# Kernel optimization log

Hardware: AMD Instinct MI355X
Metric: run time of the kernel (lower is better)

## Reference

```python
import jax, jax.numpy as jnp
import numpy as np

DIM = 128      # encoder output dim
D_OUT = 10     # num classes
T = 1.0        # temperature
EPS = 1e-7


def setup_inputs() -> dict:
    key = jax.random.key(0)
    ks = jax.random.split(key, 5)
    B, N, D_IN = 512, 100000, 128
    x = jax.random.normal(ks[0], (B, D_IN), jnp.float32)
    candidate_x = jax.random.normal(ks[1], (N, D_IN), jnp.float32)
    candidate_y = jax.random.randint(ks[2], (N,), 0, D_OUT, dtype=jnp.int32)
    W = jax.random.normal(ks[3], (DIM, D_IN), jnp.float32) / np.sqrt(D_IN).astype(np.float32)
    b = jax.random.normal(ks[4], (DIM,), jnp.float32) * 0.01
    return {"x": x, "candidate_x": candidate_x, "candidate_y": candidate_y, "W": W, "b": b}


def reference(x, candidate_x, candidate_y, W, b):
    # Linear encoder (n_blocks == 0 path)
    h = x @ W.T + b              # [B, DIM]
    hc = candidate_x @ W.T + b   # [N, DIM]
    # Pairwise L2 distances via the Gram expansion (same math as torch.cdist p=2)
    d2 = (jnp.sum(h * h, axis=-1, keepdims=True)
          + jnp.sum(hc * hc, axis=-1)[None, :]
          - 2.0 * (h @ hc.T))    # [B, N]
    dist = jnp.sqrt(jnp.maximum(d2, 0.0)) / T
    # Attention-like masked softmax over candidates (eval: no diagonal mask)
    p = jax.nn.softmax(-dist, axis=-1)              # [B, N]
    onehot_y = jax.nn.one_hot(candidate_y, D_OUT, dtype=p.dtype)  # [N, D_OUT]
    logits = p @ onehot_y                           # [B, D_OUT]
    return jnp.log(logits + EPS)
```

## Files before the change

kernel.cpp:

```cpp
#include <hip/hip_runtime.h>
#include <stdint.h>

typedef __bf16 bf16x8 __attribute__((ext_vector_type(8)));
typedef float f32x4 __attribute__((ext_vector_type(4)));
typedef short short8 __attribute__((ext_vector_type(8)));
typedef unsigned short ushort4v __attribute__((ext_vector_type(4)));
typedef float float4_t __attribute__((ext_vector_type(4)));

union FragU { short8 s; bf16x8 b; };

#define DEVI static __device__ __forceinline__

DEVI f32x4 mfma16(bf16x8 a, bf16x8 b, f32x4 c) {
  return __builtin_amdgcn_mfma_f32_16x16x32_bf16(a, b, c, 0, 0, 0);
}

DEVI bf16x8 cvt8(float4_t a, float4_t b) {
  bf16x8 r;
  r[0] = (__bf16)a[0]; r[1] = (__bf16)a[1]; r[2] = (__bf16)a[2]; r[3] = (__bf16)a[3];
  r[4] = (__bf16)b[0]; r[5] = (__bf16)b[1]; r[6] = (__bf16)b[2]; r[7] = (__bf16)b[3];
  return r;
}

__global__ __launch_bounds__(256) void setup_kernel(
    const float* __restrict__ W, unsigned short* __restrict__ Wbf,
    const int* __restrict__ y, unsigned short* __restrict__ YT,
    float* __restrict__ hcn, int N, int NP, int bpc) {
  const int bid = blockIdx.x, t = threadIdx.x;
  if (bid < 8) {
    int i = (bid * 256 + t) * 8;
    float4_t v0 = *(const float4_t*)(W + i);
    float4_t v1 = *(const float4_t*)(W + i + 4);
    FragU u; u.b = cvt8(v0, v1);
    *(short8*)(Wbf + i) = u.s;
  } else if (bid == 8) {
    int i = N + t;
    if (i < NP) hcn[i] = 1e30f;
  } else {
    int k = bid - 9;
    int c = k / bpc, j = k - c * bpc;
    int n0 = j * 2048 + t * 8;
    unsigned short* dst = YT + (size_t)c * NP + n0;
#pragma unroll
    for (int e = 0; e < 8; ++e) {
      int n = n0 + e;
      if (n < NP) dst[e] = (n < N && y[n] == c) ? 0x3F80u : 0u;
    }
  }
}

__global__ __launch_bounds__(256) void encode_kernel(
    const float* __restrict__ in, const unsigned short* __restrict__ Wbf,
    const float* __restrict__ bias, unsigned short* __restrict__ outh,
    float* __restrict__ outnorm, int M) {
  const int t = threadIdx.x, lane = t & 63, w = t >> 6;
  const int g = lane >> 4, q = lane & 15;
  const int rowbase = blockIdx.x * 64 + w * 16;

  bf16x8 a[4];
  {
    int arow = rowbase + q;
    bool v = arow < M;
    int ar = v ? arow : 0;
#pragma unroll
    for (int kc = 0; kc < 4; ++kc) {
      const float4_t* p = (const float4_t*)(in + (size_t)ar * 128 + kc * 32 + g * 8);
      float4_t v0 = p[0], v1 = p[1];
      FragU u; u.b = cvt8(v0, v1);
      if (!v) u.s = short8{0, 0, 0, 0, 0, 0, 0, 0};
      a[kc] = u.b;
    }
  }

  f32x4 acc[8];
#pragma unroll
  for (int nt = 0; nt < 8; ++nt) acc[nt] = f32x4{0.f, 0.f, 0.f, 0.f};

#pragma unroll
  for (int nt = 0; nt < 8; ++nt) {
#pragma unroll
    for (int kc = 0; kc < 4; ++kc) {
      FragU u;
      u.s = *(const short8*)(Wbf + (size_t)(nt * 16 + q) * 128 + kc * 32 + g * 8);
      acc[nt] = mfma16(a[kc], u.b, acc[nt]);
    }
  }

  float nsq[4] = {0.f, 0.f, 0.f, 0.f};
#pragma unroll
  for (int nt = 0; nt < 8; ++nt) {
    int col = nt * 16 + q;
    float bv = bias[col];
#pragma unroll
    for (int r = 0; r < 4; ++r) {
      int row = rowbase + g * 4 + r;
      float val = acc[nt][r] + bv;
      __bf16 h = (__bf16)val;
      float vf = (float)h;
      nsq[r] += vf * vf;
      union { __bf16 h; unsigned short u; } cv; cv.h = h;
      if (row < M) outh[(size_t)row * 128 + col] = cv.u;
    }
  }
#pragma unroll
  for (int m = 1; m < 16; m <<= 1) {
#pragma unroll
    for (int r = 0; r < 4; ++r) nsq[r] += __shfl_xor(nsq[r], m, 64);
  }
  if (q == 0) {
#pragma unroll
    for (int r = 0; r < 4; ++r) {
      int row = rowbase + g * 4 + r;
      if (row < M) outnorm[row] = nsq[r];
    }
  }
}

__global__ __launch_bounds__(512) void nca_main(
    const unsigned short* __restrict__ H, const float* __restrict__ hnorm,
    const unsigned short* __restrict__ HC, const float* __restrict__ hcnorm,
    const unsigned short* __restrict__ YT, float* __restrict__ gbins,
    int B, int N, int NP, int NT, int CHUNKS) {
  __shared__ __align__(16) unsigned short HCl[2][64 * 128];

  const int t = threadIdx.x, lane = t & 63, w = t >> 6;
  const int g = lane >> 4, q = lane & 15;
  const int rg = blockIdx.y, chunk = blockIdx.x;
  const int t0 = (int)(((long long)chunk * NT) / CHUNKS);
  const int t1 = (int)(((long long)(chunk + 1) * NT) / CHUNKS);
  const int rowbase = rg * 128 + w * 16;

  bf16x8 hfrag[4];
  {
    int arow = rowbase + q;
    bool v = arow < B;
    int ar = v ? arow : 0;
#pragma unroll
    for (int kc = 0; kc < 4; ++kc) {
      FragU u;
      u.s = *(const short8*)(H + (size_t)ar * 128 + kc * 32 + g * 8);
      if (!v) u.s = short8{0, 0, 0, 0, 0, 0, 0, 0};
      hfrag[kc] = u.b;
    }
  }
  const int hrow = rowbase + q;
  const float hn = hnorm[hrow < B ? hrow : 0];

  f32x4 pool = f32x4{0.f, 0.f, 0.f, 0.f};

#define STAGE(TT, BUF)                                                        \
  {                                                                           \
    _Pragma("unroll") for (int i = 0; i < 2; ++i) {                           \
      int SI = t + 512 * i;                                                   \
      int row = SI >> 4, s = SI & 15;                                         \
      int srcslot = s ^ (row & 7);                                            \
      int cg = (TT)*64 + row;                                                 \
      if (cg >= N) cg = N - 1;                                                \
      const unsigned short* src = HC + (size_t)cg * 128 + srcslot * 8;        \
      char* ldsbase = (char*)HCl[BUF] + w * 1024 + i * 8192;                  \
      __builtin_amdgcn_global_load_lds(                                       \
          (const __attribute__((address_space(1))) unsigned int*)src,         \
          (__attribute__((address_space(3))) unsigned int*)ldsbase, 16, 0, 0);\
    }                                                                         \
  }

  int cur = 0;
  if (t0 < t1) STAGE(t0, 0);

  for (int tt = t0; tt < t1; ++tt) {
    __syncthreads();
    if (tt + 1 < t1) STAGE(tt + 1, cur ^ 1);

    const int colbase = tt * 64;
    float4_t cnv[4];
    ushort4v ytv[4];
#pragma unroll
    for (int ns = 0; ns < 4; ++ns) {
      cnv[ns] = *(const float4_t*)(hcnorm + colbase + ns * 16 + g * 4);
      ytv[ns] = *(const ushort4v*)(YT + (size_t)q * NP + colbase + ns * 16 + g * 4);
    }

    f32x4 acc[4];
#pragma unroll
    for (int ns = 0; ns < 4; ++ns) acc[ns] = f32x4{0.f, 0.f, 0.f, 0.f};
#pragma unroll
    for (int ns = 0; ns < 4; ++ns) {
      int brow = ns * 16 + q;
#pragma unroll
      for (int kc = 0; kc < 4; ++kc) {
        int slot = (kc * 4 + g) ^ (brow & 7);
        FragU u;
        u.s = *(const short8*)((const char*)HCl[cur] + brow * 256 + slot * 16);
        acc[ns] = mfma16(u.b, hfrag[kc], acc[ns]);
      }
    }

#pragma unroll
    for (int ns = 0; ns < 4; ++ns) {
      FragU wb; wb.s = short8{0, 0, 0, 0, 0, 0, 0, 0};
#pragma unroll
      for (int r = 0; r < 4; ++r) {
        float d2 = fmaf(-2.f, acc[ns][r], hn + cnv[ns][r]);
        d2 = fmaxf(d2, 0.f);
        float dist = __builtin_amdgcn_sqrtf(d2);
        wb.b[r] = (__bf16)__expf(0.f - dist);
      }
      FragU yb;
      yb.s = short8{(short)ytv[ns][0], (short)ytv[ns][1],
                    (short)ytv[ns][2], (short)ytv[ns][3], 0, 0, 0, 0};
      pool = mfma16(yb.b, wb.b, pool);
    }
    cur ^= 1;
  }

  if (hrow < B) {
#pragma unroll
    for (int r = 0; r < 4; ++r) {
      int c = g * 4 + r;
      if (c < 10) atomicAdd(&gbins[hrow * 10 + c], pool[r]);
    }
  }
#undef STAGE
}

__global__ __launch_bounds__(256) void finalize_kernel(
    const float* __restrict__ gbins, float* __restrict__ out, int B) {
  int row = blockIdx.x * blockDim.x + threadIdx.x;
  if (row >= B) return;
  float s[10], Z = 0.f;
#pragma unroll
  for (int c = 0; c < 10; ++c) {
    s[c] = gbins[row * 10 + c];
    Z += s[c];
  }
  float inv = 1.f / Z;
#pragma unroll
  for (int c = 0; c < 10; ++c) out[row * 10 + c] = logf(fmaf(s[c], inv, 1e-7f));
}

extern "C" void kernel_launch(void* const* d_in, const int* in_sizes, int n_in,
                              void* d_out, int out_size, void* d_ws,
                              size_t ws_size, hipStream_t stream) {
  const float* x = (const float*)d_in[0];
  const float* cx = (const float*)d_in[1];
  const int* cy = (const int*)d_in[2];
  const float* W = (const float*)d_in[3];
  const float* b = (const float*)d_in[4];
  const int B = in_sizes[0] / 128;
  const int N = in_sizes[1] / 128;
  float* out = (float*)d_out;

  const int NT = (N + 63) / 64;
  const int NP = NT * 64;

  char* ws = (char*)d_ws;
  size_t o = 0;
  auto alloc = [&](size_t bytes) {
    size_t r = o;
    o += (bytes + 255) & ~(size_t)255;
    return r;
  };
  unsigned short* HC = (unsigned short*)(ws + alloc((size_t)N * 128 * 2));
  float* hcn = (float*)(ws + alloc((size_t)NP * 4));
  unsigned short* H = (unsigned short*)(ws + alloc((size_t)B * 128 * 2));
  float* hn = (float*)(ws + alloc((size_t)B * 4));
  float* gbins = (float*)(ws + alloc((size_t)B * 10 * 4));
  unsigned short* Wbf = (unsigned short*)(ws + alloc(128 * 128 * 2));
  unsigned short* YT = (unsigned short*)(ws + alloc((size_t)16 * NP * 2));

  (void)hipMemsetAsync(gbins, 0, (size_t)B * 10 * 4, stream);
  const int bpc = (NP + 2047) / 2048;
  setup_kernel<<<9 + 16 * bpc, 256, 0, stream>>>(W, Wbf, cy, YT, hcn, N, NP, bpc);
  encode_kernel<<<(N + 63) / 64, 256, 0, stream>>>(cx, Wbf, b, HC, hcn, N);
  encode_kernel<<<(B + 63) / 64, 256, 0, stream>>>(x, Wbf, b, H, hn, B);

  const int CHUNKS = 192;
  const int RG = (B + 127) / 128;
  dim3 grid(CHUNKS, RG);
  nca_main<<<grid, 512, 0, stream>>>(H, hn, HC, hcn, YT, gbins, B, N, NP, NT,
                                     CHUNKS);
  finalize_kernel<<<(B + 255) / 256, 256, 0, stream>>>(gbins, out, B);
}
```

Measured before the change: 201.5 us.

## Process two query row-sets per block and replace atomics with partial-sum reduction

```diff
diff --git a/kernel.cpp b/kernel.cpp
--- a/kernel.cpp
+++ b/kernel.cpp
@@ -4,10 +4,11 @@
 typedef __bf16 bf16x8 __attribute__((ext_vector_type(8)));
 typedef float f32x4 __attribute__((ext_vector_type(4)));
 typedef short short8 __attribute__((ext_vector_type(8)));
-typedef unsigned short ushort4v __attribute__((ext_vector_type(4)));
+typedef unsigned int uint2v __attribute__((ext_vector_type(2)));
 typedef float float4_t __attribute__((ext_vector_type(4)));
 
 union FragU { short8 s; bf16x8 b; };
+union YbU { uint2v u2[2]; bf16x8 b; };
 
 #define DEVI static __device__ __forceinline__
 
@@ -50,12 +51,23 @@
 }
 
 __global__ __launch_bounds__(256) void encode_kernel(
-    const float* __restrict__ in, const unsigned short* __restrict__ Wbf,
-    const float* __restrict__ bias, unsigned short* __restrict__ outh,
-    float* __restrict__ outnorm, int M) {
+    const float* __restrict__ inA, const float* __restrict__ inB,
+    const unsigned short* __restrict__ Wbf, const float* __restrict__ bias,
+    unsigned short* __restrict__ outA, float* __restrict__ normA,
+    unsigned short* __restrict__ outB, float* __restrict__ normB,
+    int MA, int MB, int NBA) {
+  const float* in;
+  unsigned short* outh;
+  float* outnorm;
+  int M, blk;
+  if ((int)blockIdx.x < NBA) {
+    in = inA; outh = outA; outnorm = normA; M = MA; blk = blockIdx.x;
+  } else {
+    in = inB; outh = outB; outnorm = normB; M = MB; blk = blockIdx.x - NBA;
+  }
   const int t = threadIdx.x, lane = t & 63, w = t >> 6;
   const int g = lane >> 4, q = lane & 15;
-  const int rowbase = blockIdx.x * 64 + w * 16;
+  const int rowbase = blk * 64 + w * 16;
 
   bf16x8 a[4];
   {
@@ -75,7 +87,6 @@
   f32x4 acc[8];
 #pragma unroll
   for (int nt = 0; nt < 8; ++nt) acc[nt] = f32x4{0.f, 0.f, 0.f, 0.f};
-
 #pragma unroll
   for (int nt = 0; nt < 8; ++nt) {
 #pragma unroll
@@ -116,11 +127,11 @@
   }
 }
 
-__global__ __launch_bounds__(512) void nca_main(
+__global__ __launch_bounds__(512, 4) void nca_main(
     const unsigned short* __restrict__ H, const float* __restrict__ hnorm,
     const unsigned short* __restrict__ HC, const float* __restrict__ hcnorm,
-    const unsigned short* __restrict__ YT, float* __restrict__ gbins,
-    int B, int N, int NP, int NT, int CHUNKS) {
+    const unsigned short* __restrict__ YT, float* __restrict__ part,
+    int B, int BP, int N, int NP, int NT, int CHUNKS) {
   __shared__ __align__(16) unsigned short HCl[2][64 * 128];
 
   const int t = threadIdx.x, lane = t & 63, w = t >> 6;
@@ -128,25 +139,27 @@
   const int rg = blockIdx.y, chunk = blockIdx.x;
   const int t0 = (int)(((long long)chunk * NT) / CHUNKS);
   const int t1 = (int)(((long long)(chunk + 1) * NT) / CHUNKS);
-  const int rowbase = rg * 128 + w * 16;
-
-  bf16x8 hfrag[4];
-  {
-    int arow = rowbase + q;
-    bool v = arow < B;
-    int ar = v ? arow : 0;
+
+  bf16x8 hfrag[2][4];
+  float hn[2];
+  int hrow[2];
+#pragma unroll
+  for (int s = 0; s < 2; ++s) {
+    hrow[s] = rg * 256 + s * 128 + w * 16 + q;
+    bool v = hrow[s] < B;
+    int ar = v ? hrow[s] : 0;
 #pragma unroll
     for (int kc = 0; kc < 4; ++kc) {
       FragU u;
       u.s = *(const short8*)(H + (size_t)ar * 128 + kc * 32 + g * 8);
       if (!v) u.s = short8{0, 0, 0, 0, 0, 0, 0, 0};
-      hfrag[kc] = u.b;
-    }
-  }
-  const int hrow = rowbase + q;
-  const float hn = hnorm[hrow < B ? hrow : 0];
-
-  f32x4 pool = f32x4{0.f, 0.f, 0.f, 0.f};
+      hfrag[s][kc] = u.b;
+    }
+    hn[s] = hnorm[ar];
+  }
+
+  f32x4 pool0 = f32x4{0.f, 0.f, 0.f, 0.f};
+  f32x4 pool1 = f32x4{0.f, 0.f, 0.f, 0.f};
 
 #define STAGE(TT, BUF)                                                        \
   {                                                                           \
@@ -173,69 +186,70 @@
 
     const int colbase = tt * 64;
     float4_t cnv[4];
-    ushort4v ytv[4];
+    uint2v ytu[4];
 #pragma unroll
     for (int ns = 0; ns < 4; ++ns) {
       cnv[ns] = *(const float4_t*)(hcnorm + colbase + ns * 16 + g * 4);
-      ytv[ns] = *(const ushort4v*)(YT + (size_t)q * NP + colbase + ns * 16 + g * 4);
-    }
-
-    f32x4 acc[4];
-#pragma unroll
-    for (int ns = 0; ns < 4; ++ns) acc[ns] = f32x4{0.f, 0.f, 0.f, 0.f};
+      ytu[ns] = *(const uint2v*)(YT + (size_t)q * NP + colbase + ns * 16 + g * 4);
+    }
+
 #pragma unroll
     for (int ns = 0; ns < 4; ++ns) {
       int brow = ns * 16 + q;
+      f32x4 a0 = f32x4{0.f, 0.f, 0.f, 0.f};
+      f32x4 a1 = f32x4{0.f, 0.f, 0.f, 0.f};
 #pragma unroll
       for (int kc = 0; kc < 4; ++kc) {
         int slot = (kc * 4 + g) ^ (brow & 7);
         FragU u;
         u.s = *(const short8*)((const char*)HCl[cur] + brow * 256 + slot * 16);
-        acc[ns] = mfma16(u.b, hfrag[kc], acc[ns]);
+        a0 = mfma16(u.b, hfrag[0][kc], a0);
+        a1 = mfma16(u.b, hfrag[1][kc], a1);
       }
-    }
-
-#pragma unroll
-    for (int ns = 0; ns < 4; ++ns) {
-      FragU wb; wb.s = short8{0, 0, 0, 0, 0, 0, 0, 0};
+      FragU wb0, wb1;
+      wb0.s = short8{0, 0, 0, 0, 0, 0, 0, 0};
+      wb1.s = short8{0, 0, 0, 0, 0, 0, 0, 0};
 #pragma unroll
       for (int r = 0; r < 4; ++r) {
-        float d2 = fmaf(-2.f, acc[ns][r], hn + cnv[ns][r]);
-        d2 = fmaxf(d2, 0.f);
-        float dist = __builtin_amdgcn_sqrtf(d2);
-        wb.b[r] = (__bf16)__expf(0.f - dist);
+        float d20 = fmaf(-2.f, a0[r], hn[0] + cnv[ns][r]);
+        float d21 = fmaf(-2.f, a1[r], hn[1] + cnv[ns][r]);
+        d20 = fmaxf(d20, 0.f);
+        d21 = fmaxf(d21, 0.f);
+        float di0 = __builtin_amdgcn_sqrtf(d20);
+        float di1 = __builtin_amdgcn_sqrtf(d21);
+        wb0.b[r] = (__bf16)__expf(0.f - di0);
+        wb1.b[r] = (__bf16)__expf(0.f - di1);
       }
-      FragU yb;
-      yb.s = short8{(short)ytv[ns][0], (short)ytv[ns][1],
-                    (short)ytv[ns][2], (short)ytv[ns][3], 0, 0, 0, 0};
-      pool = mfma16(yb.b, wb.b, pool);
+      YbU yb;
+      yb.u2[0] = ytu[ns];
+      yb.u2[1] = uint2v{0u, 0u};
+      pool0 = mfma16(yb.b, wb0.b, pool0);
+      pool1 = mfma16(yb.b, wb1.b, pool1);
     }
     cur ^= 1;
   }
-
-  if (hrow < B) {
-#pragma unroll
-    for (int r = 0; r < 4; ++r) {
-      int c = g * 4 + r;
-      if (c < 10) atomicAdd(&gbins[hrow * 10 + c], pool[r]);
-    }
-  }
 #undef STAGE
-}
-
-__global__ __launch_bounds__(256) void finalize_kernel(
-    const float* __restrict__ gbins, float* __restrict__ out, int B) {
-  int row = blockIdx.x * blockDim.x + threadIdx.x;
-  if (row >= B) return;
-  float s[10], Z = 0.f;
-#pragma unroll
-  for (int c = 0; c < 10; ++c) {
-    s[c] = gbins[row * 10 + c];
-    Z += s[c];
-  }
-  float inv = 1.f / Z;
-#pragma unroll
-  for (int c = 0; c < 10; ++c) out[row * 10 + c] = logf(fmaf(s[c], inv, 1e-7f));
+
+  if (hrow[0] < B)
+    *(f32x4*)(part + ((size_t)chunk * BP + hrow[0]) * 16 + g * 4) = pool0;
+  if (hrow[1] < B)
+    *(f32x4*)(part + ((size_t)chunk * BP + hrow[1]) * 16 + g * 4) = pool1;
+}
+
+__global__ __launch_bounds__(64) void finalize_kernel(
+    const float* __restrict__ part, float* __restrict__ out, int B, int BP,
+    int CHUNKS) {
+  const int row = blockIdx.x, t = threadIdx.x;
+  const int c = t & 15, grp = t >> 4;
+  float s = 0.f;
+  for (int j = grp; j < CHUNKS; j += 4)
+    s += part[((size_t)j * BP + row) * 16 + c];
+  s += __shfl_xor(s, 16, 64);
+  s += __shfl_xor(s, 32, 64);
+  float Z = 0.f;
+#pragma unroll
+  for (int cc = 0; cc < 10; ++cc) Z += __shfl(s, cc, 64);
+  if (t < 10) out[row * 10 + t] = logf(fmaf(s, 1.f / Z, 1e-7f));
 }
 
 extern "C" void kernel_launch(void* const* d_in, const int* in_sizes, int n_in,
@@ -252,6 +266,8 @@
 
   const int NT = (N + 63) / 64;
   const int NP = NT * 64;
+  const int RG = (B + 255) / 256;
+  const int BP = RG * 256;
 
   char* ws = (char*)d_ws;
   size_t o = 0;
@@ -264,20 +280,24 @@
   float* hcn = (float*)(ws + alloc((size_t)NP * 4));
   unsigned short* H = (unsigned short*)(ws + alloc((size_t)B * 128 * 2));
   float* hn = (float*)(ws + alloc((size_t)B * 4));
-  float* gbins = (float*)(ws + alloc((size_t)B * 10 * 4));
   unsigned short* Wbf = (unsigned short*)(ws + alloc(128 * 128 * 2));
   unsigned short* YT = (unsigned short*)(ws + alloc((size_t)16 * NP * 2));
 
-  (void)hipMemsetAsync(gbins, 0, (size_t)B * 10 * 4, stream);
+  size_t avail = (ws_size > o) ? (ws_size - o) : 0;
+  int CHUNKS = (int)(avail / ((size_t)BP * 16 * 4));
+  if (CHUNKS > 256) CHUNKS = 256;
+  if (CHUNKS < 32) CHUNKS = 32;
+  float* part = (float*)(ws + alloc((size_t)CHUNKS * BP * 16 * 4));
+
   const int bpc = (NP + 2047) / 2048;
   setup_kernel<<<9 + 16 * bpc, 256, 0, stream>>>(W, Wbf, cy, YT, hcn, N, NP, bpc);
-  encode_kernel<<<(N + 63) / 64, 256, 0, stream>>>(cx, Wbf, b, HC, hcn, N);
-  encode_kernel<<<(B + 63) / 64, 256, 0, stream>>>(x, Wbf, b, H, hn, B);
-
-  const int CHUNKS = 192;
-  const int RG = (B + 127) / 128;
+
+  const int NBA = (N + 63) / 64, NBB = (B + 63) / 64;
+  encode_kernel<<<NBA + NBB, 256, 0, stream>>>(cx, x, Wbf, b, HC, hcn, H, hn,
+                                               N, B, NBA);
+
   dim3 grid(CHUNKS, RG);
-  nca_main<<<grid, 512, 0, stream>>>(H, hn, HC, hcn, YT, gbins, B, N, NP, NT,
-                                     CHUNKS);
-  finalize_kernel<<<(B + 255) / 256, 256, 0, stream>>>(gbins, out, B);
-}
+  nca_main<<<grid, 512, 0, stream>>>(H, hn, HC, hcn, YT, part, B, BP, N, NP,
+                                     NT, CHUNKS);
+  finalize_kernel<<<B, 64, 0, stream>>>(part, out, B, BP, CHUNKS);
+}
```

After: 176.7 us. -12.3%, faster.
